# Performance work log

Hardware: AMD Instinct MI355X
Metric: run time of the kernel (lower is better)

The kernel has to match this reference:

```python
import jax, jax.numpy as jnp
import numpy as np

HIDDEN = 1280
HEADS = 16
HEAD_DIM = HIDDEN // HEADS  # 80
B, N = 2, 2048


def _rotate_half(x):
    half = x.shape[-1] // 2
    return jnp.concatenate([-x[..., half:], x[..., :half]], axis=-1)


def setup_inputs() -> dict:
    key = jax.random.key(0)
    ks = jax.random.split(key, 7)
    x = jax.random.normal(ks[0], (B, N, HIDDEN), dtype=jnp.float32)
    cos = jax.random.uniform(ks[1], (N, HEAD_DIM), dtype=jnp.float32)
    sin = jax.random.uniform(ks[2], (N, HEAD_DIM), dtype=jnp.float32)
    s = 1.0 / np.sqrt(HIDDEN)
    qkv_w = jax.random.normal(ks[3], (HIDDEN, 3 * HIDDEN), dtype=jnp.float32) * s
    qkv_b = jax.random.normal(ks[4], (3 * HIDDEN,), dtype=jnp.float32) * 0.02
    proj_w = jax.random.normal(ks[5], (HIDDEN, HIDDEN), dtype=jnp.float32) * s
    proj_b = jax.random.normal(ks[6], (HIDDEN,), dtype=jnp.float32) * 0.02
    return {"x": x, "cos": cos, "sin": sin, "qkv_w": qkv_w, "qkv_b": qkv_b,
            "proj_w": proj_w, "proj_b": proj_b}


def reference(x, cos, sin, qkv_w, qkv_b, proj_w, proj_b):
    b, n, _ = x.shape
    scale = 1.0 / np.sqrt(HEAD_DIM).astype(np.float32)
    # fused QKV projection
    qkv = x @ qkv_w + qkv_b                                # [b, n, 3*hidden]
    qkv = qkv.reshape(b, n, 3, HEADS, HEAD_DIM)
    qkv = jnp.transpose(qkv, (2, 0, 3, 1, 4))              # [3, b, h, n, hd]
    q, k, v = qkv[0], qkv[1], qkv[2]
    # 2D RoPE
    cos_b = cos[None, None, :, :]
    sin_b = sin[None, None, :, :]
    q = q * cos_b + _rotate_half(q) * sin_b
    k = k * cos_b + _rotate_half(k) * sin_b
    # manual softmax attention
    scores = jnp.einsum('bhqd,bhkd->bhqk', q, k) * scale   # [b, h, n, n]
    attn = jax.nn.softmax(scores, axis=-1)
    out = jnp.einsum('bhqk,bhkd->bhqd', attn, v)           # [b, h, n, hd]
    out = jnp.transpose(out, (0, 2, 1, 3)).reshape(b, n, HIDDEN)
    return out @ proj_w + proj_b
```

## Files before the change

kernel.cpp:

```cpp
#include <hip/hip_runtime.h>
#include <hip/hip_bf16.h>
#include <math.h>

#define HIDDEN 1280
#define HEADS 16
#define HD 80
#define HALF 40
#define BB 2
#define NN 2048
#define MROWS (BB * NN)
#define QSCALE ((float)(0.11180339887498949 * 1.4426950408889634))

typedef __attribute__((ext_vector_type(8))) _Float16 f16x8;
typedef __attribute__((ext_vector_type(4))) float f32x4;

#define AS1 __attribute__((address_space(1)))
#define AS3 __attribute__((address_space(3)))

__device__ __forceinline__ void splitf16(float x, ushort& hi, ushort& lo) {
    _Float16 h = (_Float16)x;
    _Float16 l = (_Float16)(x - (float)h);
    hi = __builtin_bit_cast(ushort, h);
    lo = __builtin_bit_cast(ushort, l);
}

__device__ __forceinline__ ushort f2h(float x) {
    _Float16 h = (_Float16)x;
    return __builtin_bit_cast(ushort, h);
}

__device__ __forceinline__ void tsplit_tile(
    const float* __restrict__ W, ushort* __restrict__ T, int K, int N,
    int n0, int k0, float (*s)[33], int tid)
{
    {
        int tn = tid & 31, tk = tid >> 5;
        #pragma unroll
        for (int i = 0; i < 4; ++i)
            s[tk + i * 8][tn] = W[(size_t)(k0 + tk + i * 8) * N + n0 + tn];
    }
    __syncthreads();
    {
        int tk = tid & 31, tn = tid >> 5;
        #pragma unroll
        for (int i = 0; i < 4; ++i)
            T[(size_t)(n0 + tn + i * 8) * K + k0 + tk] = f2h(s[tk][tn + i * 8]);
    }
}

__global__ __launch_bounds__(256) void prep_kernel(
    const float* __restrict__ x, ushort* __restrict__ a_hi,
    ushort* __restrict__ a_lo,
    const float* __restrict__ qkv_w, ushort* __restrict__ wT,
    const float* __restrict__ proj_w, ushort* __restrict__ pT)
{
    __shared__ float s[32][33];
    const int tid = threadIdx.x;
    const int id = blockIdx.x;

    if (id < 5120) {
        int i = id * 256 + tid;
        float4 v = ((const float4*)x)[i];
        ushort4 h, l;
        splitf16(v.x, h.x, l.x);
        splitf16(v.y, h.y, l.y);
        splitf16(v.z, h.z, l.z);
        splitf16(v.w, h.w, l.w);
        ((ushort4*)a_hi)[i] = h;
        ((ushort4*)a_lo)[i] = l;
    } else if (id < 9920) {
        int id2 = id - 5120;
        int n0 = (id2 % 120) * 32, k0 = (id2 / 120) * 32;
        tsplit_tile(qkv_w, wT, HIDDEN, 3 * HIDDEN, n0, k0, s, tid);
    } else {
        int id2 = id - 9920;
        int n0 = (id2 % 40) * 32, k0 = (id2 / 40) * 32;
        tsplit_tile(proj_w, pT, HIDDEN, HIDDEN, n0, k0, s, tid);
    }
}

#define BM 128
#define BN 128
#define BK 32

__global__ __launch_bounds__(256) void gemm_f16x2_kernel(
    const ushort* __restrict__ Ahi, const ushort* __restrict__ Alo,
    const ushort* __restrict__ Bh,
    const float* __restrict__ bias, float* __restrict__ C,
    int M, int N, int K)
{
    __shared__ __align__(16) ushort lds[2 * 12288];

    const int tid = threadIdx.x;
    const int wid = tid >> 6;
    const int lane = tid & 63;
    const int col0 = blockIdx.x * BN;
    const int row0 = blockIdx.y * BM;
    const int wy = wid >> 1, wx = wid & 1;
    const int lrow = lane >> 2;
    const int lchunk = lane & 3;
    const int q = lane >> 4;
    const int r = lane & 15;

    const ushort* gsrc[6];
    int ldst[6];
    #pragma unroll
    for (int i = 0; i < 6; ++i) {
        int s = wid + i * 4;
        int tile = s >> 3, t = s & 7;
        const ushort* src = (tile == 0) ? Ahi : (tile == 1) ? Alo : Bh;
        int srow = (tile < 2) ? row0 : col0;
        gsrc[i] = src + (size_t)(srow + t * 16 + lrow) * K + lchunk * 8;
        ldst[i] = tile * 4096 + t * 512 + lane * 8;
    }

    const int NT = K / BK;

    #pragma unroll
    for (int i = 0; i < 6; ++i)
        __builtin_amdgcn_global_load_lds((const AS1 unsigned int*)(gsrc[i]),
            (AS3 unsigned int*)(lds + ldst[i]), 16, 0, 0);
    asm volatile("s_waitcnt vmcnt(0)" ::: "memory");
    __builtin_amdgcn_s_barrier();

    f32x4 acc[4][4] = {};
    int cb = 0;

    for (int t = 0; t < NT; ++t) {
        const ushort* base = lds + cb;
        ushort* nbuf = lds + (12288 - cb);
        if (t + 1 < NT) {
            const int ko = (t + 1) * BK;
            #pragma unroll
            for (int i = 0; i < 6; ++i)
                __builtin_amdgcn_global_load_lds((const AS1 unsigned int*)(gsrc[i] + ko),
                    (AS3 unsigned int*)(nbuf + ldst[i]), 16, 0, 0);
        }

        f16x8 ah[4], al[4], bf[4];
        #pragma unroll
        for (int i = 0; i < 4; ++i) {
            int arow = wy * 64 + i * 16 + r;
            ah[i] = *(const f16x8*)(base + 0 * 4096 + arow * 32 + q * 8);
            al[i] = *(const f16x8*)(base + 1 * 4096 + arow * 32 + q * 8);
            int brow = wx * 64 + i * 16 + r;
            bf[i] = *(const f16x8*)(base + 2 * 4096 + brow * 32 + q * 8);
        }
        #pragma unroll
        for (int i = 0; i < 4; ++i) {
            #pragma unroll
            for (int j = 0; j < 4; ++j) {
                acc[i][j] = __builtin_amdgcn_mfma_f32_16x16x32_f16(al[i], bf[j], acc[i][j], 0, 0, 0);
                acc[i][j] = __builtin_amdgcn_mfma_f32_16x16x32_f16(ah[i], bf[j], acc[i][j], 0, 0, 0);
            }
        }

        asm volatile("s_waitcnt vmcnt(0)" ::: "memory");
        __builtin_amdgcn_s_barrier();
        cb = 12288 - cb;
    }

    #pragma unroll
    for (int i = 0; i < 4; ++i) {
        #pragma unroll
        for (int j = 0; j < 4; ++j) {
            int col = col0 + wx * 64 + j * 16 + r;
            float b = bias[col];
            #pragma unroll
            for (int v = 0; v < 4; ++v) {
                int row = row0 + wy * 64 + i * 16 + q * 4 + v;
                C[(size_t)row * N + col] = acc[i][j][v] + b;
            }
        }
    }
}

__global__ __launch_bounds__(512, 4) void gemm_f16x2_256x128_kernel(
    const ushort* __restrict__ Ahi, const ushort* __restrict__ Alo,
    const ushort* __restrict__ Bh,
    const float* __restrict__ bias, float* __restrict__ C,
    int M, int N, int K, int nbx)
{
    __shared__ __align__(16) ushort lds[2 * 20480];

    const int tid = threadIdx.x;
    const int wid = tid >> 6;
    const int lane = tid & 63;
    const int q = lane >> 4, r = lane & 15;
    const int wr = wid >> 1;
    const int wc = wid & 1;

    int id = blockIdx.x;
    {
        int nwg = gridDim.x;
        if ((nwg & 7) == 0) {
            int c = nwg >> 3;
            id = (id & 7) * c + (id >> 3);
        }
    }
    const int row0 = (id / nbx) * 256;
    const int col0 = (id % nbx) * 128;

    const ushort* gsrc[5];
    int ldst[5];
    #pragma unroll
    for (int j = 0; j < 5; ++j) {
        if (j < 4) {
            int p = j >> 1;
            int rloc = wid * 32 + (j & 1) * 16 + (lane >> 2);
            int sl = (lane & 3) ^ ((rloc >> 1) & 3);
            const ushort* base = p ? Alo : Ahi;
            gsrc[j] = base + (size_t)(row0 + rloc) * K + sl * 8;
            ldst[j] = p * 8192 + (wid * 32 + (j & 1) * 16) * 32 + lane * 8;
        } else {
            int rloc = wid * 16 + (lane >> 2);
            int sl = (lane & 3) ^ ((rloc >> 1) & 3);
            gsrc[4] = Bh + (size_t)(col0 + rloc) * K + sl * 8;
            ldst[4] = 16384 + wid * 512 + lane * 8;
        }
    }

    const int NT = K / 32;

    #pragma unroll
    for (int j = 0; j < 5; ++j)
        __builtin_amdgcn_global_load_lds((const AS1 unsigned int*)(gsrc[j]),
            (AS3 unsigned int*)(lds + ldst[j]), 16, 0, 0);
    asm volatile("s_waitcnt vmcnt(0)" ::: "memory");
    __builtin_amdgcn_s_barrier();

    const int soff = (q ^ ((r >> 1) & 3)) * 8;
    const int arow0 = wr * 64 + r;
    const int brow0 = wc * 64 + r;

    f32x4 acc[4][4] = {};
    f16x8 ah[4], al[4], bf[2];

    int cb = 0;
    for (int t = 0; t < NT; ++t) {
        const ushort* A0 = lds + cb;
        const ushort* A1 = lds + cb + 8192;
        const ushort* Bp = lds + cb + 16384;
        ushort* nbuf = lds + (20480 - cb);
        const bool st = (t + 1 < NT);
        const int ko = (t + 1) * 32;

        #pragma unroll
        for (int m = 0; m < 4; ++m) {
            int ro = (arow0 + m * 16) * 32 + soff;
            ah[m] = *(const f16x8*)(A0 + ro);
            al[m] = *(const f16x8*)(A1 + ro);
        }
        #pragma unroll
        for (int n = 0; n < 2; ++n)
            bf[n] = *(const f16x8*)(Bp + (brow0 + n * 16) * 32 + soff);
        if (st) {
            __builtin_amdgcn_global_load_lds((const AS1 unsigned int*)(gsrc[0] + ko),
                (AS3 unsigned int*)(nbuf + ldst[0]), 16, 0, 0);
            __builtin_amdgcn_global_load_lds((const AS1 unsigned int*)(gsrc[1] + ko),
                (AS3 unsigned int*)(nbuf + ldst[1]), 16, 0, 0);
            __builtin_amdgcn_global_load_lds((const AS1 unsigned int*)(gsrc[2] + ko),
                (AS3 unsigned int*)(nbuf + ldst[2]), 16, 0, 0);
        }
        __builtin_amdgcn_s_barrier();
        asm volatile("s_waitcnt lgkmcnt(0)" ::: "memory");
        __builtin_amdgcn_sched_barrier(0);
        __builtin_amdgcn_s_setprio(1);
        #pragma unroll
        for (int m = 0; m < 4; ++m) {
            #pragma unroll
            for (int n = 0; n < 2; ++n) {
                acc[m][n] = __builtin_amdgcn_mfma_f32_16x16x32_f16(al[m], bf[n], acc[m][n], 0, 0, 0);
                acc[m][n] = __builtin_amdgcn_mfma_f32_16x16x32_f16(ah[m], bf[n], acc[m][n], 0, 0, 0);
            }
        }
        __builtin_amdgcn_s_setprio(0);
        __builtin_amdgcn_s_barrier();

        #pragma unroll
        for (int n = 0; n < 2; ++n)
            bf[n] = *(const f16x8*)(Bp + (brow0 + (n + 2) * 16) * 32 + soff);
        if (st) {
            __builtin_amdgcn_global_load_lds((const AS1 unsigned int*)(gsrc[3] + ko),
                (AS3 unsigned int*)(nbuf + ldst[3]), 16, 0, 0);
            __builtin_amdgcn_global_load_lds((const AS1 unsigned int*)(gsrc[4] + ko),
                (AS3 unsigned int*)(nbuf + ldst[4]), 16, 0, 0);
        }
        __builtin_amdgcn_s_barrier();
        asm volatile("s_waitcnt lgkmcnt(0)" ::: "memory");
        __builtin_amdgcn_sched_barrier(0);
        __builtin_amdgcn_s_setprio(1);
        #pragma unroll
        for (int m = 0; m < 4; ++m) {
            #pragma unroll
            for (int n = 0; n < 2; ++n) {
                acc[m][n + 2] = __builtin_amdgcn_mfma_f32_16x16x32_f16(al[m], bf[n], acc[m][n + 2], 0, 0, 0);
                acc[m][n + 2] = __builtin_amdgcn_mfma_f32_16x16x32_f16(ah[m], bf[n], acc[m][n + 2], 0, 0, 0);
            }
        }
        __builtin_amdgcn_s_setprio(0);
        asm volatile("s_waitcnt vmcnt(0)" ::: "memory");
        __builtin_amdgcn_s_barrier();
        cb = 20480 - cb;
    }

    #pragma unroll
    for (int m = 0; m < 4; ++m) {
        #pragma unroll
        for (int n = 0; n < 4; ++n) {
            int col = col0 + wc * 64 + n * 16 + r;
            float b = bias[col];
            #pragma unroll
            for (int v = 0; v < 4; ++v) {
                int row = row0 + wr * 64 + m * 16 + q * 4 + v;
                C[(size_t)row * N + col] = acc[m][n][v] + b;
            }
        }
    }
}

__global__ __launch_bounds__(256) void rope_split_kernel(
    const float* __restrict__ qkv, const float* __restrict__ cos_t,
    const float* __restrict__ sin_t,
    ushort* __restrict__ qf, ushort* __restrict__ kf,
    ushort* __restrict__ vt)
{
    __shared__ float s_v[64][84];
    const int tid = threadIdx.x;
    const int b = blockIdx.z, h = blockIdx.y;
    const int n0 = blockIdx.x * 64;
    const int bh = b * HEADS + h;

    #pragma unroll
    for (int i = 0; i < 5; ++i) {
        int u = tid + i * 256;
        int n = u / 20, c = u % 20;
        const float* src = qkv + (size_t)(b * NN + n0 + n) * 3840 + 2 * HIDDEN + h * HD + c * 4;
        *(float4*)(&s_v[n][c * 4]) = *(const float4*)src;
    }

    for (int u = tid; u < 640; u += 256) {
        int n = u / 10, p = u % 10;
        int d = p * 4;
        int ng = n0 + n;
        size_t rowb = (size_t)(b * NN + ng) * 3840;
        float4 c0 = *(const float4*)(cos_t + ng * HD + d);
        float4 c1 = *(const float4*)(cos_t + ng * HD + d + HALF);
        float4 s0 = *(const float4*)(sin_t + ng * HD + d);
        float4 s1 = *(const float4*)(sin_t + ng * HD + d + HALF);
        size_t qo = ((size_t)bh * NN + ng) * 96;
        {
            float4 x0 = *(const float4*)(qkv + rowb + h * HD + d);
            float4 x1 = *(const float4*)(qkv + rowb + h * HD + d + HALF);
            ushort4 h4a, h4b;
            h4a.x = f2h((x0.x * c0.x - x1.x * s0.x) * QSCALE);
            h4a.y = f2h((x0.y * c0.y - x1.y * s0.y) * QSCALE);
            h4a.z = f2h((x0.z * c0.z - x1.z * s0.z) * QSCALE);
            h4a.w = f2h((x0.w * c0.w - x1.w * s0.w) * QSCALE);
            h4b.x = f2h((x1.x * c1.x + x0.x * s1.x) * QSCALE);
            h4b.y = f2h((x1.y * c1.y + x0.y * s1.y) * QSCALE);
            h4b.z = f2h((x1.z * c1.z + x0.z * s1.z) * QSCALE);
            h4b.w = f2h((x1.w * c1.w + x0.w * s1.w) * QSCALE);
            *(ushort4*)(qf + qo + d) = h4a;
            *(ushort4*)(qf + qo + d + HALF) = h4b;
        }
        {
            float4 x0 = *(const float4*)(qkv + rowb + HIDDEN + h * HD + d);
            float4 x1 = *(const float4*)(qkv + rowb + HIDDEN + h * HD + d + HALF);
            ushort4 h4a, h4b;
            h4a.x = f2h(x0.x * c0.x - x1.x * s0.x);
            h4a.y = f2h(x0.y * c0.y - x1.y * s0.y);
            h4a.z = f2h(x0.z * c0.z - x1.z * s0.z);
            h4a.w = f2h(x0.w * c0.w - x1.w * s0.w);
            h4b.x = f2h(x1.x * c1.x + x0.x * s1.x);
            h4b.y = f2h(x1.y * c1.y + x0.y * s1.y);
            h4b.z = f2h(x1.z * c1.z + x0.z * s1.z);
            h4b.w = f2h(x1.w * c1.w + x0.w * s1.w);
            *(ushort4*)(kf + qo + d) = h4a;
            *(ushort4*)(kf + qo + d + HALF) = h4b;
        }
    }

    {
        int which = tid >> 7;
        int u = tid & 127;
        int n = u >> 1, part = u & 1;
        size_t o = ((size_t)bh * NN + n0 + n) * 96 + 80 + part * 8;
        uint4 z = {0u, 0u, 0u, 0u};
        if (which == 0) *(uint4*)(qf + o) = z;
        else            *(uint4*)(kf + o) = z;
    }
    __syncthreads();

    for (int u = tid; u < 320; u += 256) {
        int d = u >> 2, nc = u & 3;
        ushort hs[16];
        #pragma unroll
        for (int kk = 0; kk < 16; ++kk)
            hs[kk] = f2h(s_v[nc * 16 + kk][d]);
        size_t o = ((size_t)bh * HD + d) * NN + n0 + nc * 16;
        uint4 w0, w1;
        w0.x = (uint)hs[0] | ((uint)hs[1] << 16);
        w0.y = (uint)hs[2] | ((uint)hs[3] << 16);
        w0.z = (uint)hs[4] | ((uint)hs[5] << 16);
        w0.w = (uint)hs[6] | ((uint)hs[7] << 16);
        w1.x = (uint)hs[8] | ((uint)hs[9] << 16);
        w1.y = (uint)hs[10] | ((uint)hs[11] << 16);
        w1.z = (uint)hs[12] | ((uint)hs[13] << 16);
        w1.w = (uint)hs[14] | ((uint)hs[15] << 16);
        *(uint4*)(vt + o) = w0;
        *(uint4*)(vt + o + 8) = w1;
    }
}

__global__ __launch_bounds__(512, 2) void attn_mfma_kernel(
    const ushort* __restrict__ qf, const ushort* __restrict__ kf,
    const ushort* __restrict__ vt,
    ushort* __restrict__ ao_hi, ushort* __restrict__ ao_lo)
{
    __shared__ __align__(16) ushort lds[43008];
    ushort* p_s = lds + 26624;

    const int tid = threadIdx.x;
    const int wave = tid >> 6, lane = tid & 63;
    const int quad = lane >> 4, r = lane & 15;
    const int b = blockIdx.z, h = blockIdx.y;
    const int bh = b * HEADS + h;
    const int q0 = blockIdx.x * 256;

    const size_t kb = (size_t)bh * NN * 96;
    const size_t vb = (size_t)bh * HD * NN;

    const ushort* gptr[4];
    int ldso[4];
    #pragma unroll
    for (int i = 0; i < 4; ++i) {
        int s = wave + i * 8;
        if (s < 16) {
            int row = s * 4 + (lane >> 4);
            int t = lane & 15;
            int g = t ^ (row & 7);
            if (g >= 12) g = 0;
            gptr[i] = kf + kb + (size_t)row * 96 + g * 8;
            ldso[i] = s * 512 + lane * 8;
        } else if (s < 26) {
            int ts = s - 16;
            gptr[i] = vt + vb + (size_t)(ts * 8 + (lane >> 3)) * NN
                      + (size_t)(((lane & 7) ^ (lane >> 3)) * 8);
            ldso[i] = 8192 + ts * 512 + lane * 8;
        } else {
            gptr[i] = nullptr;
            ldso[i] = 0;
        }
    }

    f16x8 qfr[2][3];
    #pragma unroll
    for (int mt = 0; mt < 2; ++mt)
        #pragma unroll
        for (int c = 0; c < 3; ++c) {
            size_t o = ((size_t)bh * NN + q0 + wave * 32 + mt * 16 + r) * 96 + c * 32 + quad * 8;
            qfr[mt][c] = *(const f16x8*)(qf + o);
        }

    f32x4 oacc[2][5] = {};
    float l_lane[2] = {0.0f, 0.0f};

    const int prow0 = (wave * 32 + r) * 64;
    const int prow1 = (wave * 32 + 16 + r) * 64;
    const int r7 = r & 7;

    #pragma unroll
    for (int i = 0; i < 4; ++i) {
        int s = wave + i * 8;
        if (s < 26) {
            __builtin_amdgcn_global_load_lds((const AS1 unsigned int*)gptr[i],
                (AS3 unsigned int*)(lds + ldso[i]), 16, 0, 0);
            gptr[i] += (s < 16) ? 6144 : 64;
        }
    }
    asm volatile("s_waitcnt vmcnt(0)" ::: "memory");
    __builtin_amdgcn_s_barrier();

    int cur = 0;
    for (int j0 = 0; j0 < NN; j0 += 64) {
        const int nxt = 13312 - cur;
        if (j0 + 64 < NN) {
            #pragma unroll
            for (int i = 0; i < 4; ++i) {
                int s = wave + i * 8;
                if (s < 26) {
                    __builtin_amdgcn_global_load_lds((const AS1 unsigned int*)gptr[i],
                        (AS3 unsigned int*)(lds + nxt + ldso[i]), 16, 0, 0);
                    gptr[i] += (s < 16) ? 6144 : 64;
                }
            }
        }

        const ushort* k_s = lds + cur;
        const _Float16* v_s = (const _Float16*)(lds + cur + 8192);

        f32x4 sc[2][4] = {};
        __builtin_amdgcn_s_setprio(1);
        #pragma unroll
        for (int jt = 0; jt < 4; ++jt) {
            f16x8 kbf[3];
            int j = jt * 16 + r;
            #pragma unroll
            for (int c = 0; c < 3; ++c) {
                int ch = (c * 4 + quad) ^ r7;
                kbf[c] = *(const f16x8*)(k_s + j * 128 + ch * 8);
            }
            #pragma unroll
            for (int c = 0; c < 3; ++c) {
                sc[0][jt] = __builtin_amdgcn_mfma_f32_16x16x32_f16(kbf[c], qfr[0][c], sc[0][jt], 0, 0, 0);
                sc[1][jt] = __builtin_amdgcn_mfma_f32_16x16x32_f16(kbf[c], qfr[1][c], sc[1][jt], 0, 0, 0);
            }
        }
        __builtin_amdgcn_s_setprio(0);

        #pragma unroll
        for (int mt = 0; mt < 2; ++mt) {
            const int prow = mt ? prow1 : prow0;
            #pragma unroll
            for (int jt = 0; jt < 4; ++jt) {
                float p0 = __builtin_amdgcn_exp2f(sc[mt][jt][0]);
                float p1 = __builtin_amdgcn_exp2f(sc[mt][jt][1]);
                float p2 = __builtin_amdgcn_exp2f(sc[mt][jt][2]);
                float p3 = __builtin_amdgcn_exp2f(sc[mt][jt][3]);
                l_lane[mt] += p0;
                l_lane[mt] += p1;
                l_lane[mt] += p2;
                l_lane[mt] += p3;
                uint2 w;
                w.x = (uint)f2h(p0) | ((uint)f2h(p1) << 16);
                w.y = (uint)f2h(p2) | ((uint)f2h(p3) << 16);
                int off = prow + (((jt * 2 + (quad >> 1)) ^ r7) * 8) + (quad & 1) * 4;
                *(uint2*)(p_s + off) = w;
            }
        }

        f16x8 pa[2][2];
        #pragma unroll
        for (int cc = 0; cc < 2; ++cc) {
            int gp = ((cc * 4 + quad) ^ r7) * 8;
            pa[0][cc] = *(const f16x8*)(p_s + prow0 + gp);
            pa[1][cc] = *(const f16x8*)(p_s + prow1 + gp);
        }

        __builtin_amdgcn_s_setprio(1);
        #pragma unroll
        for (int dt = 0; dt < 5; ++dt)
            #pragma unroll
            for (int cc = 0; cc < 2; ++cc) {
                int ck = (cc * 4 + quad) ^ r7;
                f16x8 vbf = *(const f16x8*)(v_s + (dt * 16 + r) * 64 + ck * 8);
                oacc[0][dt] = __builtin_amdgcn_mfma_f32_16x16x32_f16(pa[0][cc], vbf, oacc[0][dt], 0, 0, 0);
                oacc[1][dt] = __builtin_amdgcn_mfma_f32_16x16x32_f16(pa[1][cc], vbf, oacc[1][dt], 0, 0, 0);
            }
        __builtin_amdgcn_s_setprio(0);

        asm volatile("s_waitcnt vmcnt(0)" ::: "memory");
        __builtin_amdgcn_s_barrier();
        cur = nxt;
    }

    float inv_l[2][4];
    #pragma unroll
    for (int mt = 0; mt < 2; ++mt) {
        float lt = l_lane[mt];
        lt += __shfl_xor(lt, 16);
        lt += __shfl_xor(lt, 32);
        #pragma unroll
        for (int v = 0; v < 4; ++v)
            inv_l[mt][v] = 1.0f / __shfl(lt, quad * 4 + v);
    }

    __syncthreads();
    #pragma unroll
    for (int mt = 0; mt < 2; ++mt)
        #pragma unroll
        for (int v = 0; v < 4; ++v) {
            int row = wave * 32 + mt * 16 + quad * 4 + v;
            #pragma unroll
            for (int dt = 0; dt < 5; ++dt) {
                float o = oacc[mt][dt][v] * inv_l[mt][v];
                ushort hh, ll;
                splitf16(o, hh, ll);
                lds[row * 80 + dt * 16 + r] = hh;
                lds[20480 + row * 80 + dt * 16 + r] = ll;
            }
        }
    __syncthreads();
    {
        size_t gbase = ((size_t)b * NN + q0) * HIDDEN + h * HD;
        #pragma unroll
        for (int i = 0; i < 10; ++i) {
            int u = tid + i * 512;
            int plane = u / 2560, idx = u % 2560;
            int row = idx / 10, part = idx % 10;
            uint4 w = *(const uint4*)(lds + plane * 20480 + idx * 8);
            ushort* dst = (plane ? ao_lo : ao_hi) + gbase + (size_t)row * HIDDEN + part * 8;
            *(uint4*)dst = w;
        }
    }
}

extern "C" void kernel_launch(void* const* d_in, const int* in_sizes, int n_in,
                              void* d_out, int out_size, void* d_ws, size_t ws_size,
                              hipStream_t stream)
{
    const float* x      = (const float*)d_in[0];
    const float* cos_t  = (const float*)d_in[1];
    const float* sin_t  = (const float*)d_in[2];
    const float* qkv_w  = (const float*)d_in[3];
    const float* qkv_b  = (const float*)d_in[4];
    const float* proj_w = (const float*)d_in[5];
    const float* proj_b = (const float*)d_in[6];
    float* out = (float*)d_out;

    char* ws = (char*)d_ws;
    float*  qkv   = (float*)ws;
    ushort* ao_hi = (ushort*)ws;
    ushort* ao_lo = (ushort*)(ws + 10485760);
    ushort* wT    = (ushort*)(ws + 62914560);
    ushort* vt    = (ushort*)(ws + 62914560);
    ushort* a_hi  = (ushort*)(ws + 82575360);
    ushort* a_lo  = (ushort*)(ws + 93061120);
    ushort* q_f   = (ushort*)(ws + 83886080);
    ushort* k_f   = (ushort*)(ws + 96468992);
    ushort* pT    = (ushort*)(ws + 109051904);

    prep_kernel<<<dim3(11520), 256, 0, stream>>>(
        x, a_hi, a_lo, qkv_w, wT, proj_w, pT);

    gemm_f16x2_256x128_kernel<<<dim3((MROWS / 256) * (3 * HIDDEN / 128)), 512, 0, stream>>>(
        a_hi, a_lo, wT, qkv_b, qkv, MROWS, 3 * HIDDEN, HIDDEN, 3 * HIDDEN / 128);

    rope_split_kernel<<<dim3(NN / 64, HEADS, BB), 256, 0, stream>>>(
        qkv, cos_t, sin_t, q_f, k_f, vt);

    attn_mfma_kernel<<<dim3(NN / 256, HEADS, BB), 512, 0, stream>>>(
        q_f, k_f, vt, ao_hi, ao_lo);

    gemm_f16x2_kernel<<<dim3(HIDDEN / BN, MROWS / BM), 256, 0, stream>>>(
        ao_hi, ao_lo, pT, proj_b, out, MROWS, HIDDEN, HIDDEN);
}
```

Before: 301.6 us.

## Retile QKV GEMM to 128x256 with 4 waves and single-phase pipeline

Switches the QKV projection GEMM from 256x128 tiles with 8 waves to 128x256 tiles with 4 waves, each wave computing a 64x128 sub-tile with 32 accumulators. The two half-step phases with four barriers per k-step are merged into one phase: all prefetch loads are issued first, then one full set of MFMAs runs, with a single barrier at the end. This is meant to cut barrier and synchronisation overhead and raise MFMA work per LDS read. It costs many more registers per wave (the accumulators double), lower wave count per block, and a grid of 480 blocks instead of 480 with different per-block shape.

```diff
diff --git a/kernel.cpp b/kernel.cpp
--- a/kernel.cpp
+++ b/kernel.cpp
@@ -175,13 +175,13 @@
     }
 }
 
-__global__ __launch_bounds__(512, 4) void gemm_f16x2_256x128_kernel(
+__global__ __launch_bounds__(256, 2) void gemm_f16x2_128x256_kernel(
     const ushort* __restrict__ Ahi, const ushort* __restrict__ Alo,
     const ushort* __restrict__ Bh,
     const float* __restrict__ bias, float* __restrict__ C,
     int M, int N, int K, int nbx)
 {
-    __shared__ __align__(16) ushort lds[2 * 20480];
+    __shared__ __align__(16) ushort lds[2 * 16384];
 
     const int tid = threadIdx.x;
     const int wid = tid >> 6;
@@ -198,53 +198,57 @@
             id = (id & 7) * c + (id >> 3);
         }
     }
-    const int row0 = (id / nbx) * 256;
-    const int col0 = (id % nbx) * 128;
-
-    const ushort* gsrc[5];
-    int ldst[5];
-    #pragma unroll
-    for (int j = 0; j < 5; ++j) {
-        if (j < 4) {
-            int p = j >> 1;
-            int rloc = wid * 32 + (j & 1) * 16 + (lane >> 2);
-            int sl = (lane & 3) ^ ((rloc >> 1) & 3);
-            const ushort* base = p ? Alo : Ahi;
-            gsrc[j] = base + (size_t)(row0 + rloc) * K + sl * 8;
-            ldst[j] = p * 8192 + (wid * 32 + (j & 1) * 16) * 32 + lane * 8;
-        } else {
-            int rloc = wid * 16 + (lane >> 2);
-            int sl = (lane & 3) ^ ((rloc >> 1) & 3);
-            gsrc[4] = Bh + (size_t)(col0 + rloc) * K + sl * 8;
-            ldst[4] = 16384 + wid * 512 + lane * 8;
-        }
+    const int row0 = (id / nbx) * 128;
+    const int col0 = (id % nbx) * 256;
+
+    const ushort* gsrc[8];
+    int ldst[8];
+    #pragma unroll
+    for (int i = 0; i < 8; ++i) {
+        int s = wid + i * 4;
+        const ushort* srcb;
+        int t, rbase;
+        int dof;
+        if (s < 8)       { srcb = Ahi; t = s;      rbase = row0; dof = 0; }
+        else if (s < 16) { srcb = Alo; t = s - 8;  rbase = row0; dof = 4096; }
+        else             { srcb = Bh;  t = s - 16; rbase = col0; dof = 8192; }
+        int rloc = t * 16 + (lane >> 2);
+        int sl = (lane & 3) ^ ((rloc >> 1) & 3);
+        gsrc[i] = srcb + (size_t)(rbase + rloc) * K + sl * 8;
+        ldst[i] = dof + t * 512 + lane * 8;
     }
 
     const int NT = K / 32;
 
     #pragma unroll
-    for (int j = 0; j < 5; ++j)
-        __builtin_amdgcn_global_load_lds((const AS1 unsigned int*)(gsrc[j]),
-            (AS3 unsigned int*)(lds + ldst[j]), 16, 0, 0);
+    for (int i = 0; i < 8; ++i)
+        __builtin_amdgcn_global_load_lds((const AS1 unsigned int*)(gsrc[i]),
+            (AS3 unsigned int*)(lds + ldst[i]), 16, 0, 0);
     asm volatile("s_waitcnt vmcnt(0)" ::: "memory");
     __builtin_amdgcn_s_barrier();
 
     const int soff = (q ^ ((r >> 1) & 3)) * 8;
     const int arow0 = wr * 64 + r;
-    const int brow0 = wc * 64 + r;
-
-    f32x4 acc[4][4] = {};
-    f16x8 ah[4], al[4], bf[2];
-
+    const int brow0 = wc * 128 + r;
+
+    f32x4 acc[4][8] = {};
     int cb = 0;
+
     for (int t = 0; t < NT; ++t) {
         const ushort* A0 = lds + cb;
-        const ushort* A1 = lds + cb + 8192;
-        const ushort* Bp = lds + cb + 16384;
-        ushort* nbuf = lds + (20480 - cb);
-        const bool st = (t + 1 < NT);
-        const int ko = (t + 1) * 32;
-
+        const ushort* A1 = lds + cb + 4096;
+        const ushort* Bp = lds + cb + 8192;
+        ushort* nbuf = lds + (16384 - cb);
+
+        if (t + 1 < NT) {
+            const int ko = (t + 1) * 32;
+            #pragma unroll
+            for (int i = 0; i < 8; ++i)
+                __builtin_amdgcn_global_load_lds((const AS1 unsigned int*)(gsrc[i] + ko),
+                    (AS3 unsigned int*)(nbuf + ldst[i]), 16, 0, 0);
+        }
+
+        f16x8 ah[4], al[4], bf[8];
         #pragma unroll
         for (int m = 0; m < 4; ++m) {
             int ro = (arow0 + m * 16) * 32 + soff;
@@ -252,63 +256,30 @@
             al[m] = *(const f16x8*)(A1 + ro);
         }
         #pragma unroll
-        for (int n = 0; n < 2; ++n)
+        for (int n = 0; n < 8; ++n)
             bf[n] = *(const f16x8*)(Bp + (brow0 + n * 16) * 32 + soff);
-        if (st) {
-            __builtin_amdgcn_global_load_lds((const AS1 unsigned int*)(gsrc[0] + ko),
-                (AS3 unsigned int*)(nbuf + ldst[0]), 16, 0, 0);
-            __builtin_amdgcn_global_load_lds((const AS1 unsigned int*)(gsrc[1] + ko),
-                (AS3 unsigned int*)(nbuf + ldst[1]), 16, 0, 0);
-            __builtin_amdgcn_global_load_lds((const AS1 unsigned int*)(gsrc[2] + ko),
-                (AS3 unsigned int*)(nbuf + ldst[2]), 16, 0, 0);
-        }
-        __builtin_amdgcn_s_barrier();
-        asm volatile("s_waitcnt lgkmcnt(0)" ::: "memory");
-        __builtin_amdgcn_sched_barrier(0);
+
         __builtin_amdgcn_s_setprio(1);
         #pragma unroll
         for (int m = 0; m < 4; ++m) {
             #pragma unroll
-            for (int n = 0; n < 2; ++n) {
+            for (int n = 0; n < 8; ++n) {
                 acc[m][n] = __builtin_amdgcn_mfma_f32_16x16x32_f16(al[m], bf[n], acc[m][n], 0, 0, 0);
                 acc[m][n] = __builtin_amdgcn_mfma_f32_16x16x32_f16(ah[m], bf[n], acc[m][n], 0, 0, 0);
             }
         }
         __builtin_amdgcn_s_setprio(0);
-        __builtin_amdgcn_s_barrier();
-
-        #pragma unroll
-        for (int n = 0; n < 2; ++n)
-            bf[n] = *(const f16x8*)(Bp + (brow0 + (n + 2) * 16) * 32 + soff);
-        if (st) {
-            __builtin_amdgcn_global_load_lds((const AS1 unsigned int*)(gsrc[3] + ko),
-                (AS3 unsigned int*)(nbuf + ldst[3]), 16, 0, 0);
-            __builtin_amdgcn_global_load_lds((const AS1 unsigned int*)(gsrc[4] + ko),
-                (AS3 unsigned int*)(nbuf + ldst[4]), 16, 0, 0);
-        }
-        __builtin_amdgcn_s_barrier();
-        asm volatile("s_waitcnt lgkmcnt(0)" ::: "memory");
-        __builtin_amdgcn_sched_barrier(0);
-        __builtin_amdgcn_s_setprio(1);
-        #pragma unroll
-        for (int m = 0; m < 4; ++m) {
-            #pragma unroll
-            for (int n = 0; n < 2; ++n) {
-                acc[m][n + 2] = __builtin_amdgcn_mfma_f32_16x16x32_f16(al[m], bf[n], acc[m][n + 2], 0, 0, 0);
-                acc[m][n + 2] = __builtin_amdgcn_mfma_f32_16x16x32_f16(ah[m], bf[n], acc[m][n + 2], 0, 0, 0);
-            }
-        }
-        __builtin_amdgcn_s_setprio(0);
+
         asm volatile("s_waitcnt vmcnt(0)" ::: "memory");
         __builtin_amdgcn_s_barrier();
-        cb = 20480 - cb;
+        cb = 16384 - cb;
     }
 
     #pragma unroll
     for (int m = 0; m < 4; ++m) {
         #pragma unroll
-        for (int n = 0; n < 4; ++n) {
-            int col = col0 + wc * 64 + n * 16 + r;
+        for (int n = 0; n < 8; ++n) {
+            int col = col0 + wc * 128 + n * 16 + r;
             float b = bias[col];
             #pragma unroll
             for (int v = 0; v < 4; ++v) {
@@ -634,8 +605,8 @@
     prep_kernel<<<dim3(11520), 256, 0, stream>>>(
         x, a_hi, a_lo, qkv_w, wT, proj_w, pT);
 
-    gemm_f16x2_256x128_kernel<<<dim3((MROWS / 256) * (3 * HIDDEN / 128)), 512, 0, stream>>>(
-        a_hi, a_lo, wT, qkv_b, qkv, MROWS, 3 * HIDDEN, HIDDEN, 3 * HIDDEN / 128);
+    gemm_f16x2_128x256_kernel<<<dim3((MROWS / 128) * (3 * HIDDEN / 256)), 256, 0, stream>>>(
+        a_hi, a_lo, wT, qkv_b, qkv, MROWS, 3 * HIDDEN, HIDDEN, 3 * HIDDEN / 256);
 
     rope_split_kernel<<<dim3(NN / 64, HEADS, BB), 256, 0, stream>>>(
         qkv, cos_t, sin_t, q_f, k_f, vt);
```

Measured after the change: 300.6 us (median of 2 runs). No clear change (-0.3%).
